# Kernel tuning notes

Hardware: AMD Instinct MI355X
Metric: run time of the kernel (lower is better)

Reference implementation:

```python
import jax, jax.numpy as jnp
import numpy as np

N, C = 8192, 64

def setup_inputs() -> dict:
    key = jax.random.key(0)
    k1, k2, k3 = jax.random.split(key, 3)
    values = jax.random.normal(k1, (N, C), dtype=jnp.float32)
    coords = jax.random.uniform(k2, (N, 2), dtype=jnp.float32)
    spacing = jax.random.uniform(k3, (2,), dtype=jnp.float32)
    shift = jnp.zeros((2,), dtype=jnp.float32)
    return {"values": values, "coords": coords, "spacing": spacing, "shift": shift}


def reference(values, coords, spacing, shift):
    # grid_mode branch of upsample_nn: 3 shifted copies of the coord grid
    x, y = coords[:, 0], coords[:, 1]
    new_coords = jnp.concatenate([
        jnp.stack((x + spacing[0], y + spacing[1]), axis=1),
        jnp.stack((x, y + spacing[1]), axis=1),
        jnp.stack((x + spacing[0], y), axis=1),
    ], axis=0)  # [3N, 2]

    # Diffs = ||(new_coords - shift)[:,None] - coords[None,:]||, argmin over coords.
    # argmin of the L2 norm == argmin of the squared distance, so use the
    # expanded form to avoid materializing the [3N, N, 2] difference tensor.
    a = new_coords - shift  # [3N, 2]
    d2 = (jnp.sum(a * a, axis=1)[:, None]
          + jnp.sum(coords * coords, axis=1)[None, :]
          - 2.0 * a @ coords.T)  # [3N, N]
    idx = jnp.argmin(d2, axis=1)  # [3N]
    new_values = values[idx]      # [3N, C]

    out_values = jnp.concatenate([values, new_values], axis=0)   # [4N, C]
    out_coords = jnp.concatenate([coords, new_coords], axis=0)   # [4N, 2]
    return out_values, out_coords
```

## Files before the change

### kernel.cpp

```cpp
#include <hip/hip_runtime.h>

#pragma clang fp contract(off)

#define N_PTS 8192
#define C_DIM 64
#define NQ (3 * N_PTS)
#define G 64
#define NCELL (G * G)
#define MARGIN 1.2e-5f
#define HCELL (1.0f / 64.0f)
#define QBLOCKS (NQ / 32)
#define STRIPEBLKS 16
#define CPS (NCELL / STRIPEBLKS)
#define COPYBLKS 128


__device__ __forceinline__ unsigned int fsortkey(float f) {
    const unsigned int u = __float_as_uint(f);
    return (u & 0x80000000u) ? ~u : (u | 0x80000000u);
}
__device__ __forceinline__ float finvkey(unsigned int e) {
    const unsigned int u = (e & 0x80000000u) ? (e & 0x7fffffffu) : ~e;
    return __uint_as_float(u);
}

__device__ __forceinline__ void shift_query(int g, float x, float y,
                                            float sx, float sy,
                                            float& nx, float& ny) {
    if (g == 0)      { nx = x + sx; ny = y + sy; }
    else if (g == 1) { nx = x;      ny = y + sy; }
    else             { nx = x + sx; ny = y; }
}

__global__ __launch_bounds__(1024) void build_copy_kernel(
    const float2* __restrict__ coords2,
    const float4* __restrict__ values4,
    float4* __restrict__ sorted,
    int* __restrict__ starts,
    float4* __restrict__ out_values4,
    float2* __restrict__ out_coords)
{
#pragma clang fp contract(off)
    const int t = threadIdx.x;
    if (blockIdx.x >= STRIPEBLKS) {
        const int row = ((int)blockIdx.x - STRIPEBLKS) * 64 + (t >> 4);
        const int c4  = t & 15;
        out_values4[row * 16 + c4] = values4[row * 16 + c4];
        if (c4 == 0) out_coords[row] = coords2[row];
        return;
    }

    __shared__ unsigned int lhist[CPS];
    __shared__ unsigned int wred[16];
    __shared__ unsigned int wsum2[4];
    __shared__ unsigned int baseSh;

    const int b      = blockIdx.x;
    const int myBase = b * CPS;
    const int lane   = t & 63;
    const int w      = t >> 6;

    if (t < CPS) lhist[t] = 0u;
    __syncthreads();

    float2 cpt[8];
    int    cell[8];
    int cnt = 0;
    #pragma unroll
    for (int k = 0; k < 8; ++k) {
        const int i = t + 1024 * k;
        const float2 c = coords2[i];
        cpt[k] = c;
        int cx = (int)(c.x * 64.0f); cx = min(max(cx, 0), G - 1);
        int cy = (int)(c.y * 64.0f); cy = min(max(cy, 0), G - 1);
        cell[k] = cy * G + cx;
        cnt += (cell[k] < myBase) ? 1 : 0;
        const int lc = cell[k] - myBase;
        if (lc >= 0 && lc < CPS) atomicAdd(&lhist[lc], 1u);
    }

    int cv = cnt;
    #pragma unroll
    for (int s = 32; s >= 1; s >>= 1) cv += __shfl_xor(cv, s, 64);
    if (lane == 0) wred[w] = (unsigned)cv;
    __syncthreads();
    if (t == 0) {
        unsigned s = 0;
        #pragma unroll
        for (int j = 0; j < 16; ++j) s += wred[j];
        baseSh = s;
    }
    __syncthreads();
    const unsigned base = baseSh;

    unsigned h = 0, v = 0;
    if (t < CPS) {
        h = lhist[t];
        v = h;
        #pragma unroll
        for (int s = 1; s < 64; s <<= 1) {
            const unsigned o = __shfl_up(v, s, 64);
            if (lane >= s) v += o;
        }
        if (lane == 63) wsum2[w] = v;
    }
    __syncthreads();
    if (t < CPS) {
        unsigned woff = 0;
        for (int j = 0; j < w; ++j) woff += wsum2[j];
        const unsigned excl = base + woff + v - h;
        starts[myBase + t] = (int)excl;
        lhist[t] = excl;
    }
    if (b == 0 && t == 0) starts[NCELL] = N_PTS;
    __syncthreads();

    #pragma unroll
    for (int k = 0; k < 8; ++k) {
        const int lc = cell[k] - myBase;
        if (lc >= 0 && lc < CPS) {
            const unsigned pos = atomicAdd(&lhist[lc], 1u);
            const float p0 = cpt[k].x * cpt[k].x;
            const float p1 = cpt[k].y * cpt[k].y;
            const float sc = p0 + p1;
            const int i = t + 1024 * k;
            sorted[pos] = make_float4(cpt[k].x, cpt[k].y, sc, __int_as_float(i));
        }
    }
}

__global__ __launch_bounds__(256) void query_kernel(
    const float4* __restrict__ sorted,
    const int* __restrict__ starts,
    const float4* __restrict__ values4,
    const float* __restrict__ spacing,
    const float* __restrict__ shift,
    float4* __restrict__ out_values4,
    float2* __restrict__ out_coords)
{
#pragma clang fp contract(off)
    __shared__ int s_starts[NCELL + 1];

    const int tid  = threadIdx.x;
    const int lane = tid & 7;
    const int q    = blockIdx.x * 32 + (tid >> 3);
    const int g    = q >> 13;
    const int k    = q & (N_PTS - 1);

    const float4 me = sorted[k];

    for (int i = tid; i <= NCELL; i += 256) s_starts[i] = starts[i];

    const int b = __float_as_int(me.w);
    float nx, ny;
    shift_query(g, me.x, me.y, spacing[0], spacing[1], nx, ny);
    const float ax = nx - shift[0];
    const float ay = ny - shift[1];
    const float sa = (ax * ax) + (ay * ay);

    int cx = (int)floorf(ax * 64.0f); cx = min(max(cx, 0), G - 1);
    int cy = (int)floorf(ay * 64.0f); cy = min(max(cy, 0), G - 1);
    const float dxo = fmaxf(fmaxf(ax - 1.0f, -ax), 0.0f);

    __syncthreads();

    float best = INFINITY;
    int   bi   = 0x7fffffff;

#define EVAL_SPAN(S, E)                                                     \
    for (int i = (S) + lane; i < (E); i += 8) {                             \
        const float4 pt = sorted[i];                                        \
        const float p   = ax * pt.x;                                        \
        const float dv  = __builtin_fmaf(ay, pt.y, p);                      \
        const float t1  = sa + pt.z;                                        \
        const float d2  = t1 - (2.0f * dv);                                 \
        const int   j   = __float_as_int(pt.w);                             \
        if (d2 < best || (d2 == best && j < bi)) { best = d2; bi = j; }     \
    }

    const int xa = max(cx - 1, 0), xb = min(cx + 1, G - 1);
    const int ya = max(cy - 1, 0), yb = min(cy + 1, G - 1);
    int ss1[3], ee1[3];
    #pragma unroll
    for (int r = 0; r < 3; ++r) {
        const int yy = ya + r;
        const bool vv = (yy <= yb);
        ss1[r] = vv ? s_starts[yy * G + xa] : 0;
        ee1[r] = vv ? s_starts[yy * G + xb + 1] : 0;
    }
    #pragma unroll
    for (int r = 0; r < 3; ++r) {
        EVAL_SPAN(ss1[r], ee1[r])
    }

    unsigned long long key =
        ((unsigned long long)fsortkey(best) << 32) | (unsigned int)bi;
    #pragma unroll
    for (int m = 1; m < 8; m <<= 1) {
        const unsigned long long o = __shfl_xor(key, m, 8);
        if (o < key) key = o;
    }
    best = finvkey((unsigned int)(key >> 32));
    bi   = (int)(unsigned int)key;

    const float U = best + MARGIN;

    float sr = sqrtf(fmaxf(U - dxo * dxo, 0.0f));
    sr = fminf(sr, 4.0f);
    const int ylo = max((int)floorf((ay - sr) * 64.0f), 0);
    const int yhi = min((int)floorf((ay + sr) * 64.0f), G - 1);

    float scw = fminf(sqrtf(U), 4.0f);
    const int xlo_c = max((int)floorf((ax - scw) * 64.0f), 0);
    const int xhi_c = min((int)floorf((ax + scw) * 64.0f), G - 1);

    const bool skip = (ylo >= ya) && (yhi <= yb) && (xlo_c >= xa) && (xhi_c <= xb);

    if (!skip) {
        for (int yy0 = ylo; yy0 <= yhi; yy0 += 4) {
            int ss2[4], ee2[4];
            #pragma unroll
            for (int r = 0; r < 4; ++r) {
                const int yy = yy0 + r;
                bool vv = (yy <= yhi);
                const float ry0 = (float)yy * HCELL;
                const float vy  = fmaxf(fmaxf(ay - ry0 - HCELL, ry0 - ay), 0.0f);
                const float r2  = U - vy * vy;
                vv = vv && (r2 >= 0.0f);
                const float s = fminf(sqrtf(fmaxf(r2, 0.0f)), 4.0f);
                int xl = max((int)floorf((ax - s) * 64.0f), 0);
                int xh = min((int)floorf((ax + s) * 64.0f), G - 1);
                vv = vv && (xl <= xh);
                vv = vv && !(yy >= ya && yy <= yb && xl >= xa && xh <= xb);
                ss2[r] = vv ? s_starts[yy * G + xl] : 0;
                ee2[r] = vv ? s_starts[yy * G + xh + 1] : 0;
            }
            #pragma unroll
            for (int r = 0; r < 4; ++r) {
                EVAL_SPAN(ss2[r], ee2[r])
            }
        }
        key = ((unsigned long long)fsortkey(best) << 32) | (unsigned int)bi;
        #pragma unroll
        for (int m = 1; m < 8; m <<= 1) {
            const unsigned long long o = __shfl_xor(key, m, 8);
            if (o < key) key = o;
        }
        bi = (int)(unsigned int)key;
    }
#undef EVAL_SPAN

    const int qi  = g * N_PTS + b;
    const int row = N_PTS + qi;
    out_values4[row * 16 + 2 * lane + 0] = values4[bi * 16 + 2 * lane + 0];
    out_values4[row * 16 + 2 * lane + 1] = values4[bi * 16 + 2 * lane + 1];
    if (lane == 0) out_coords[row] = make_float2(nx, ny);
}

extern "C" void kernel_launch(void* const* d_in, const int* in_sizes, int n_in,
                              void* d_out, int out_size, void* d_ws, size_t ws_size,
                              hipStream_t stream)
{
    const float* values  = (const float*)d_in[0];
    const float* coords  = (const float*)d_in[1];
    const float* spacing = (const float*)d_in[2];
    const float* shift   = (const float*)d_in[3];

    float* out_values = (float*)d_out;
    float2* out_coords = (float2*)(out_values + (size_t)4 * N_PTS * C_DIM);

    char* ws = (char*)d_ws;
    float4* sorted = (float4*)ws;
    int* starts    = (int*)(ws + 131072);

    build_copy_kernel<<<STRIPEBLKS + COPYBLKS, 1024, 0, stream>>>(
        (const float2*)coords, (const float4*)values,
        sorted, starts, (float4*)out_values, out_coords);

    query_kernel<<<QBLOCKS, 256, 0, stream>>>(
        sorted, starts, (const float4*)values, spacing, shift,
        (float4*)out_values, out_coords);
}
```

Before: 23.56 us.

## Stage block's candidate grid rows into LDS before nearest-neighbor search

Result: slower. 29.66 us (+25.9%).

```diff
diff --git a/kernel.cpp b/kernel.cpp
--- a/kernel.cpp
+++ b/kernel.cpp
@@ -13,6 +13,7 @@
 #define STRIPEBLKS 16
 #define CPS (NCELL / STRIPEBLKS)
 #define COPYBLKS 128
+#define MAXPTS 2048
 
 
 __device__ __forceinline__ unsigned int fsortkey(float f) {
@@ -139,13 +140,17 @@
     float2* __restrict__ out_coords)
 {
 #pragma clang fp contract(off)
-    __shared__ int s_starts[NCELL + 1];
+    __shared__ int    s_starts[NCELL + 1];
+    __shared__ float4 s_pts[MAXPTS];
+    __shared__ int    s_cyLo, s_cyHi;
 
     const int tid  = threadIdx.x;
     const int lane = tid & 7;
     const int q    = blockIdx.x * 32 + (tid >> 3);
     const int g    = q >> 13;
     const int k    = q & (N_PTS - 1);
+
+    if (tid == 0) { s_cyLo = G; s_cyHi = -1; }
 
     const float4 me = sorted[k];
 
@@ -163,13 +168,28 @@
     const float dxo = fmaxf(fmaxf(ax - 1.0f, -ax), 0.0f);
 
     __syncthreads();
+    atomicMin(&s_cyLo, cy);
+    atomicMax(&s_cyHi, cy);
+    __syncthreads();
+
+    const int rowLo = max(s_cyLo - 1, 0);
+    const int rowHi = min(s_cyHi + 1, G - 1);
+    const int cbase = s_starts[rowLo * G];
+    const int cend  = s_starts[(rowHi + 1) * G];
+    const int clen  = cend - cbase;
+    const bool fits = (clen <= MAXPTS);
+
+    if (fits) {
+        for (int j = tid; j < clen; j += 256) s_pts[j] = sorted[cbase + j];
+    }
+    __syncthreads();
 
     float best = INFINITY;
     int   bi   = 0x7fffffff;
 
-#define EVAL_SPAN(S, E)                                                     \
-    for (int i = (S) + lane; i < (E); i += 8) {                             \
-        const float4 pt = sorted[i];                                        \
+#define EVAL_BODY(PT)                                                       \
+    {                                                                       \
+        const float4 pt = (PT);                                             \
         const float p   = ax * pt.x;                                        \
         const float dv  = __builtin_fmaf(ay, pt.y, p);                      \
         const float t1  = sa + pt.z;                                        \
@@ -177,20 +197,15 @@
         const int   j   = __float_as_int(pt.w);                             \
         if (d2 < best || (d2 == best && j < bi)) { best = d2; bi = j; }     \
     }
+#define EVAL_L(S, E) for (int i = (S) + lane; i < (E); i += 8) EVAL_BODY(s_pts[i - cbase])
+#define EVAL_G(S, E) for (int i = (S) + lane; i < (E); i += 8) EVAL_BODY(sorted[i])
 
     const int xa = max(cx - 1, 0), xb = min(cx + 1, G - 1);
     const int ya = max(cy - 1, 0), yb = min(cy + 1, G - 1);
-    int ss1[3], ee1[3];
-    #pragma unroll
-    for (int r = 0; r < 3; ++r) {
-        const int yy = ya + r;
-        const bool vv = (yy <= yb);
-        ss1[r] = vv ? s_starts[yy * G + xa] : 0;
-        ee1[r] = vv ? s_starts[yy * G + xb + 1] : 0;
-    }
-    #pragma unroll
-    for (int r = 0; r < 3; ++r) {
-        EVAL_SPAN(ss1[r], ee1[r])
+    for (int yy = ya; yy <= yb; ++yy) {
+        const int s = s_starts[yy * G + xa];
+        const int e = s_starts[yy * G + xb + 1];
+        if (fits) { EVAL_L(s, e); } else { EVAL_G(s, e); }
     }
 
     unsigned long long key =
@@ -217,28 +232,20 @@
     const bool skip = (ylo >= ya) && (yhi <= yb) && (xlo_c >= xa) && (xhi_c <= xb);
 
     if (!skip) {
-        for (int yy0 = ylo; yy0 <= yhi; yy0 += 4) {
-            int ss2[4], ee2[4];
-            #pragma unroll
-            for (int r = 0; r < 4; ++r) {
-                const int yy = yy0 + r;
-                bool vv = (yy <= yhi);
-                const float ry0 = (float)yy * HCELL;
-                const float vy  = fmaxf(fmaxf(ay - ry0 - HCELL, ry0 - ay), 0.0f);
-                const float r2  = U - vy * vy;
-                vv = vv && (r2 >= 0.0f);
-                const float s = fminf(sqrtf(fmaxf(r2, 0.0f)), 4.0f);
-                int xl = max((int)floorf((ax - s) * 64.0f), 0);
-                int xh = min((int)floorf((ax + s) * 64.0f), G - 1);
-                vv = vv && (xl <= xh);
-                vv = vv && !(yy >= ya && yy <= yb && xl >= xa && xh <= xb);
-                ss2[r] = vv ? s_starts[yy * G + xl] : 0;
-                ee2[r] = vv ? s_starts[yy * G + xh + 1] : 0;
-            }
-            #pragma unroll
-            for (int r = 0; r < 4; ++r) {
-                EVAL_SPAN(ss2[r], ee2[r])
-            }
+        for (int yy = ylo; yy <= yhi; ++yy) {
+            const float ry0 = (float)yy * HCELL;
+            const float vy  = fmaxf(fmaxf(ay - ry0 - HCELL, ry0 - ay), 0.0f);
+            const float r2  = U - vy * vy;
+            if (r2 < 0.0f) continue;
+            const float s = fminf(sqrtf(r2), 4.0f);
+            const int xl = max((int)floorf((ax - s) * 64.0f), 0);
+            const int xh = min((int)floorf((ax + s) * 64.0f), G - 1);
+            if (xl > xh) continue;
+            if (yy >= ya && yy <= yb && xl >= xa && xh <= xb) continue;
+            const int ss = s_starts[yy * G + xl];
+            const int ee = s_starts[yy * G + xh + 1];
+            if (fits && yy >= rowLo && yy <= rowHi) { EVAL_L(ss, ee); }
+            else                                    { EVAL_G(ss, ee); }
         }
         key = ((unsigned long long)fsortkey(best) << 32) | (unsigned int)bi;
         #pragma unroll
@@ -248,12 +255,15 @@
         }
         bi = (int)(unsigned int)key;
     }
-#undef EVAL_SPAN
-
+#undef EVAL_L
+#undef EVAL_G
+#undef EVAL_BODY
+
+    bi = min(max(bi, 0), N_PTS - 1);
     const int qi  = g * N_PTS + b;
     const int row = N_PTS + qi;
-    out_values4[row * 16 + 2 * lane + 0] = values4[bi * 16 + 2 * lane + 0];
-    out_values4[row * 16 + 2 * lane + 1] = values4[bi * 16 + 2 * lane + 1];
+    out_values4[row * 16 + lane]     = values4[bi * 16 + lane];
+    out_values4[row * 16 + 8 + lane] = values4[bi * 16 + 8 + lane];
     if (lane == 0) out_coords[row] = make_float2(nx, ny);
 }
 
```
